# Performance work log

Measured on AMD Instinct MI355X. Metric: run time of the kernel, lower is better.

The kernel has to match this reference:

```python
import jax, jax.numpy as jnp
import numpy as np

NUM_HEADS = 8


def setup_inputs() -> dict:
    key = jax.random.key(0)
    ks = jax.random.split(key, 7)
    B, H, W, C = 1, 64, 64, 512
    x = jax.random.normal(ks[0], (B, H, W, C), dtype=jnp.float32)
    # lat in [-pi/2, pi/2), lon in [0, 2*pi) radians
    lat_grid = (jax.random.uniform(ks[1], (H, W), dtype=jnp.float32) - 0.5) * np.float32(np.pi)
    lon_grid = jax.random.uniform(ks[2], (H, W), dtype=jnp.float32) * np.float32(2 * np.pi)
    w_qkv = jax.random.normal(ks[3], (3 * C, C), dtype=jnp.float32) * 0.02
    b_qkv = jax.random.normal(ks[4], (3 * C,), dtype=jnp.float32) * 0.02
    w_out = jax.random.normal(ks[5], (C, C), dtype=jnp.float32) * 0.02
    b_out = jax.random.normal(ks[6], (C,), dtype=jnp.float32) * 0.02
    return {"x": x, "lat_grid": lat_grid, "lon_grid": lon_grid,
            "w_qkv": w_qkv, "b_qkv": b_qkv, "w_out": w_out, "b_out": b_out}


def _distance_bias(lat_grid, lon_grid):
    # Haversine great-circle distance between all pairs of grid points.
    lat = lat_grid.reshape(-1)  # [N]
    lon = lon_grid.reshape(-1)
    dlat = lat[None, :] - lat[:, None]  # [N, N]
    dlon = lon[None, :] - lon[:, None]
    a = jnp.sin(dlat / 2) ** 2 + jnp.cos(lat)[:, None] * jnp.cos(lat)[None, :] * jnp.sin(dlon / 2) ** 2
    dist = 2.0 * jnp.arcsin(jnp.sqrt(jnp.clip(a, 0.0, 1.0)))
    # torch .std() is unbiased (ddof=1)
    return -dist / jnp.std(dist, ddof=1)


def reference(x, lat_grid, lon_grid, w_qkv, b_qkv, w_out, b_out):
    B, H, W, C = x.shape
    nh = NUM_HEADS
    dh = C // nh
    N = H * W
    qkv = x @ w_qkv.T + b_qkv  # [B, H, W, 3C]
    qkv = qkv.reshape(B, N, 3, nh, dh)
    q = jnp.transpose(qkv[:, :, 0], (0, 2, 1, 3))  # [B, nh, N, dh]
    k = jnp.transpose(qkv[:, :, 1], (0, 2, 1, 3))
    v = jnp.transpose(qkv[:, :, 2], (0, 2, 1, 3))
    scale = np.float32(1.0 / np.sqrt(dh))
    attn = jnp.einsum("bhnd,bhmd->bhnm", q, k) * scale  # [B, nh, N, N]
    attn = attn + _distance_bias(lat_grid, lon_grid)[None, None]
    attn = jax.nn.softmax(attn, axis=-1)  # dropout is identity in eval
    out = jnp.einsum("bhnm,bhmd->bhnd", attn, v)  # [B, nh, N, dh]
    out = jnp.transpose(out, (0, 2, 1, 3)).reshape(B, H, W, C)
    return out @ w_out.T + b_out
```

## Files before the change

### kernel.cpp

```cpp
#include <hip/hip_runtime.h>
#include <hip/hip_bf16.h>


typedef __attribute__((ext_vector_type(8))) short bf16x8;
typedef __attribute__((ext_vector_type(4))) float f32x4;

#define MFMA16(a, b, c) __builtin_amdgcn_mfma_f32_16x16x32_bf16(a, b, c, 0, 0, 0)

__device__ __forceinline__ unsigned short f2b(float f) {
    union { float f; unsigned int i; } v;
    v.f = f;
    unsigned int lsb = (v.i >> 16) & 1u;
    unsigned int r = v.i + 0x7fffu + lsb;
    return (unsigned short)(r >> 16);
}

__global__ __launch_bounds__(256) void cvt_frag(
    const float* __restrict__ in, unsigned short* __restrict__ out) {
    int t = blockIdx.x * 256 + threadIdx.x;
    int l = t & 15, qd = (t >> 4) & 3, c = (t >> 6) & 15, g = t >> 10;
    const float* src = in + ((size_t)g * 16 + l) * 512 + c * 32 + qd * 8;
    float4 v0 = *(const float4*)src;
    float4 v1 = *(const float4*)(src + 4);
    ushort4 u0, u1;
    u0.x = f2b(v0.x); u0.y = f2b(v0.y); u0.z = f2b(v0.z); u0.w = f2b(v0.w);
    u1.x = f2b(v1.x); u1.y = f2b(v1.y); u1.z = f2b(v1.z); u1.w = f2b(v1.w);
    unsigned short* dst = out + (size_t)t * 8;
    *(ushort4*)dst = u0;
    *(ushort4*)(dst + 4) = u1;
}

__global__ __launch_bounds__(256) void dist_kernel(
    const float* __restrict__ lat, const float* __restrict__ lon,
    float* __restrict__ dist, double* __restrict__ partials) {
    __shared__ float sl_i[64], sc_i[64], so_i[64];
    __shared__ float sl_j[64], sc_j[64], so_j[64];
    __shared__ double rs[256], rs2[256];

    int bi = blockIdx.x;
    int i0 = (bi >> 6) << 6;
    int j0 = (bi & 63) << 6;
    int tid = threadIdx.x;

    if (tid < 64) {
        float la = lat[i0 + tid];
        sl_i[tid] = la; sc_i[tid] = __cosf(la); so_i[tid] = lon[i0 + tid];
    } else if (tid < 128) {
        int t = tid - 64;
        float la = lat[j0 + t];
        sl_j[t] = la; sc_j[t] = __cosf(la); so_j[t] = lon[j0 + t];
    }
    __syncthreads();

    double s = 0.0, s2 = 0.0;
    int col = tid & 63;
    int pcol = ((col & 15) << 2) + (col >> 4);
    float latj = sl_j[col], cj = sc_j[col], lonj = so_j[col];
#pragma unroll
    for (int kk = 0; kk < 16; kk++) {
        int row = (kk << 2) + (tid >> 6);
        float dlat = latj - sl_i[row];
        float dlon = lonj - so_i[row];
        float h1 = __sinf(0.5f * dlat);
        float h2 = __sinf(0.5f * dlon);
        float a = h1 * h1 + sc_i[row] * cj * h2 * h2;
        a = fminf(fmaxf(a, 0.0f), 1.0f);
        float d = 2.0f * asinf(sqrtf(a));
        dist[(size_t)(i0 + row) * 4096 + j0 + pcol] = d;
        s += (double)d;
        s2 += (double)d * (double)d;
    }
    rs[tid] = s; rs2[tid] = s2;
    __syncthreads();
    for (int off = 128; off > 0; off >>= 1) {
        if (tid < off) { rs[tid] += rs[tid + off]; rs2[tid] += rs2[tid + off]; }
        __syncthreads();
    }
    if (tid == 0) {
        partials[2 * bi] = rs[0];
        partials[2 * bi + 1] = rs2[0];
    }
}

__global__ __launch_bounds__(256) void stats_kernel(
    const double* __restrict__ partials, float* __restrict__ neg_inv_std) {
    __shared__ double rs[256], rs2[256];
    int tid = threadIdx.x;
    double s = 0.0, s2 = 0.0;
    for (int i = tid; i < 4096; i += 256) {
        s += partials[2 * i];
        s2 += partials[2 * i + 1];
    }
    rs[tid] = s; rs2[tid] = s2;
    __syncthreads();
    for (int off = 128; off > 0; off >>= 1) {
        if (tid < off) { rs[tid] += rs[tid + off]; rs2[tid] += rs2[tid + off]; }
        __syncthreads();
    }
    if (tid == 0) {
        double n = 16777216.0;
        double mean = rs[0] / n;
        double var = (rs2[0] - n * mean * mean) / (n - 1.0);
        *neg_inv_std = (float)(-1.0 / sqrt(var));
    }
}

__global__ __launch_bounds__(256) void qkv_gemm(
    const unsigned short* __restrict__ x, const unsigned short* __restrict__ w,
    const float* __restrict__ b,
    unsigned short* __restrict__ q, unsigned short* __restrict__ k,
    unsigned short* __restrict__ vt) {
    __shared__ unsigned short stage[64][72];
    int lane = threadIdx.x & 63, wave = threadIdx.x >> 6;
    int l16 = lane & 15, quad = lane >> 4;
    int m0 = blockIdx.y * 64 + wave * 16;
    int n0 = blockIdx.x * 64;

    const unsigned short* abase = x + (size_t)(blockIdx.y * 4 + wave) * 8192 + lane * 8;
    f32x4 acc[4];
#pragma unroll
    for (int nb = 0; nb < 4; nb++) acc[nb] = (f32x4){0.f, 0.f, 0.f, 0.f};

    for (int k0 = 0; k0 < 512; k0 += 32) {
        bf16x8 af = *(const bf16x8*)(abase + (k0 >> 5) * 512);
#pragma unroll
        for (int nb = 0; nb < 4; nb++) {
            bf16x8 bf = *(const bf16x8*)(w + (size_t)((n0 >> 4) + nb) * 8192
                                           + (k0 >> 5) * 512 + lane * 8);
            acc[nb] = MFMA16(af, bf, acc[nb]);
        }
    }
    if (blockIdx.x < 8) {
#pragma unroll
        for (int nb = 0; nb < 4; nb++) {
            int j = n0 + nb * 16 + l16;
            float bj = b[j];
            int h = j >> 6, d = j & 63;
#pragma unroll
            for (int r = 0; r < 4; r++) {
                int n = m0 + quad * 4 + r;
                q[((size_t)h * 4096 + n) * 64 + d] = f2b((acc[nb][r] + bj) * 0.125f);
            }
        }
    } else if (blockIdx.x < 16) {
        int h = blockIdx.x - 8;
#pragma unroll
        for (int nb = 0; nb < 4; nb++) {
            int d = nb * 16 + l16;
            float bj = b[512 + h * 64 + d];
#pragma unroll
            for (int r = 0; r < 4; r++)
                stage[wave * 16 + quad * 4 + r][d] = f2b(acc[nb][r] + bj);
        }
        __syncthreads();
        unsigned short* kb = k + ((size_t)h << 18) + (size_t)blockIdx.y * 4096;
#pragma unroll
        for (int p = 0; p < 2; p++) {
            int rid = p * 256 + threadIdx.x;
            int t = rid >> 7;
            int rem = rid & 127;
            int half = rem >> 6, qd = (rem >> 4) & 3, l = rem & 15;
            const unsigned short* src = &stage[t * 16 + l][half * 32 + qd * 8];
            unsigned short* dst = kb + t * 1024 + half * 512 + qd * 128 + l * 8;
            *(uint4*)dst = *(const uint4*)src;
        }
    } else {
        int h = blockIdx.x - 16;
#pragma unroll
        for (int nb = 0; nb < 4; nb++) {
            int d = nb * 16 + l16;
            float bj = b[1024 + h * 64 + d];
#pragma unroll
            for (int r = 0; r < 4; r++)
                stage[d][quad * 16 + r * 4 + wave] = f2b(acc[nb][r] + bj);
        }
        __syncthreads();
        int t = threadIdx.x;
        int d = t >> 2;
        int nq = (t & 3) * 16;
        unsigned short* dst = vt + ((size_t)h << 18) + (size_t)blockIdx.y * 4096
                            + (d >> 4) * 1024 + ((nq >> 5) & 1) * 512
                            + ((nq >> 3) & 3) * 128 + (d & 15) * 8;
        const unsigned short* src = &stage[d][nq];
        *(uint4*)dst = *(const uint4*)src;
        *(uint4*)(dst + 128) = *(const uint4*)(src + 8);
    }
}

__device__ __forceinline__ void attn_step(
    const unsigned short* __restrict__ kptr, const unsigned short* __restrict__ vtp,
    short* __restrict__ pb, int h, int kv0, int lane, int l16, int quad,
    bf16x8 qf0, bf16x8 qf1, float4 (&dv)[4], const float* __restrict__ drow,
    int kv_next, float nis, f32x4 (&o)[4], float (&lam)[4]) {
    size_t tbase = ((size_t)h << 18) + ((size_t)kv0 << 6) + lane * 8;
    const unsigned short* kb = kptr + tbase;
    const unsigned short* vb = vtp + tbase;
    f32x4 s[4];
#pragma unroll
    for (int cb = 0; cb < 4; cb++) {
        bf16x8 kf0 = *(const bf16x8*)(kb + cb * 1024);
        bf16x8 kf1 = *(const bf16x8*)(kb + cb * 1024 + 512);
        f32x4 z = (f32x4){0.f, 0.f, 0.f, 0.f};
        z = MFMA16(qf0, kf0, z);
        z = MFMA16(qf1, kf1, z);
        s[cb] = z;
    }
#pragma unroll
    for (int r = 0; r < 4; r++) {
        s[0][r] = fmaf(dv[r].x, nis, s[0][r]);
        s[1][r] = fmaf(dv[r].y, nis, s[1][r]);
        s[2][r] = fmaf(dv[r].z, nis, s[2][r]);
        s[3][r] = fmaf(dv[r].w, nis, s[3][r]);
    }
#pragma unroll
    for (int r = 0; r < 4; r++)
        dv[r] = *(const float4*)(drow + (size_t)r * 4096 + kv_next);
#pragma unroll
    for (int r = 0; r < 4; r++) {
        float p0 = __expf(s[0][r]);
        float p1 = __expf(s[1][r]);
        float p2 = __expf(s[2][r]);
        float p3 = __expf(s[3][r]);
        lam[r] += (p0 + p1) + (p2 + p3);
        unsigned int w0 = (unsigned int)f2b(p0) | ((unsigned int)f2b(p1) << 16);
        unsigned int w1 = (unsigned int)f2b(p2) | ((unsigned int)f2b(p3) << 16);
        uint2 pk; pk.x = w0; pk.y = w1;
        *(uint2*)(pb + (quad * 4 + r) * 72 + l16 * 4) = pk;
    }
    bf16x8 pf0 = *(const bf16x8*)(pb + l16 * 72 + quad * 8);
    bf16x8 pf1 = *(const bf16x8*)(pb + l16 * 72 + 32 + quad * 8);
#pragma unroll
    for (int db = 0; db < 4; db++) {
        bf16x8 vf0 = *(const bf16x8*)(vb + db * 1024);
        bf16x8 vf1 = *(const bf16x8*)(vb + db * 1024 + 512);
        o[db] = MFMA16(pf0, vf0, o[db]);
        o[db] = MFMA16(pf1, vf1, o[db]);
    }
}

__global__ __launch_bounds__(256, 6) void attn_kernel(
    const unsigned short* __restrict__ q, const unsigned short* __restrict__ k,
    const unsigned short* __restrict__ vt, const float* __restrict__ dist,
    const float* __restrict__ nis_p, unsigned short* __restrict__ att) {
    __shared__ __align__(16) char smem[9216];
    int tid = threadIdx.x;
    int lane = tid & 63, wave = tid >> 6;
    int l16 = lane & 15, quad = lane >> 4;
    int b = blockIdx.x;
    int h  = b & 7;
    int qs = b >> 3;
    int qt = wave;
    int q0 = qs * 16;
    int kvbase = qt * 1024;
    float nis = *nis_p;

    short* pb = (short*)smem + wave * 1152;

    const unsigned short* qbase = q + ((size_t)h * 4096 + q0 + l16) * 64 + quad * 8;
    bf16x8 qf0 = *(const bf16x8*)(qbase);
    bf16x8 qf1 = *(const bf16x8*)(qbase + 32);

    f32x4 o[4];
    float lam[4];
#pragma unroll
    for (int r = 0; r < 4; r++) {
        lam[r] = 0.f;
        o[0][r] = 0.f; o[1][r] = 0.f; o[2][r] = 0.f; o[3][r] = 0.f;
    }

    const float* drow = dist + (size_t)(q0 + quad * 4) * 4096 + l16 * 4;
    float4 dv[4];
#pragma unroll
    for (int r = 0; r < 4; r++)
        dv[r] = *(const float4*)(drow + (size_t)r * 4096 + kvbase);

    for (int it = 0; it < 16; ++it) {
        int kv0 = kvbase + it * 64;
        int kvn = (it == 15) ? kvbase : kv0 + 64;
        attn_step(k, vt, pb, h, kv0, lane, l16, quad, qf0, qf1, dv, drow, kvn,
                  nis, o, lam);
    }

#pragma unroll
    for (int r = 0; r < 4; r++)
#pragma unroll
        for (int off = 1; off < 16; off <<= 1)
            lam[r] += __shfl_xor(lam[r], off, 64);

    __syncthreads();
    float* obuf = (float*)smem;
    float* lbuf = (float*)(smem + 4096);
    if (l16 == 0)
#pragma unroll
        for (int r = 0; r < 4; r++)
            lbuf[qt * 16 + quad * 4 + r] = lam[r];
    if (qt == 0) {
#pragma unroll
        for (int db = 0; db < 4; db++)
#pragma unroll
            for (int r = 0; r < 4; r++)
                obuf[(quad * 4 + r) * 64 + db * 16 + l16] = o[db][r];
    }
    __syncthreads();
    if (qt == 1) {
#pragma unroll
        for (int db = 0; db < 4; db++)
#pragma unroll
            for (int r = 0; r < 4; r++)
                obuf[(quad * 4 + r) * 64 + db * 16 + l16] += o[db][r];
    }
    __syncthreads();
    if (qt == 2) {
#pragma unroll
        for (int db = 0; db < 4; db++)
#pragma unroll
            for (int r = 0; r < 4; r++)
                obuf[(quad * 4 + r) * 64 + db * 16 + l16] += o[db][r];
    }
    __syncthreads();
    if (qt == 3) {
#pragma unroll
        for (int db = 0; db < 4; db++)
#pragma unroll
            for (int r = 0; r < 4; r++)
                obuf[(quad * 4 + r) * 64 + db * 16 + l16] += o[db][r];
    }
    __syncthreads();

    int rl = tid >> 4;
    int d4 = (tid & 15) * 4;
    float L = lbuf[rl] + lbuf[16 + rl] + lbuf[32 + rl] + lbuf[48 + rl];
    float rinv = 1.0f / L;
    const float* ob = obuf + rl * 64 + d4;
    ushort4 ua;
    ua.x = f2b(ob[0] * rinv); ua.y = f2b(ob[1] * rinv);
    ua.z = f2b(ob[2] * rinv); ua.w = f2b(ob[3] * rinv);
    int row = q0 + rl;
    int col = h * 64 + d4;
    size_t dst = (size_t)(row >> 4) * 8192 + (col >> 5) * 512
               + ((col >> 3) & 3) * 128 + (row & 15) * 8 + (col & 7);
    *(ushort4*)(att + dst) = ua;
}

__global__ __launch_bounds__(256) void out_gemm(
    const unsigned short* __restrict__ att, const unsigned short* __restrict__ w,
    const float* __restrict__ b, float* __restrict__ out) {
    int lane = threadIdx.x & 63, wave = threadIdx.x >> 6;
    int l16 = lane & 15, quad = lane >> 4;
    int m0 = blockIdx.y * 64 + wave * 16;
    int n0 = blockIdx.x * 64;

    const unsigned short* abase = att + (size_t)(blockIdx.y * 4 + wave) * 8192 + lane * 8;
    f32x4 acc[4];
#pragma unroll
    for (int nb = 0; nb < 4; nb++) acc[nb] = (f32x4){0.f, 0.f, 0.f, 0.f};

    for (int k0 = 0; k0 < 512; k0 += 32) {
        bf16x8 af = *(const bf16x8*)(abase + (k0 >> 5) * 512);
#pragma unroll
        for (int nb = 0; nb < 4; nb++) {
            bf16x8 bf = *(const bf16x8*)(w + (size_t)((n0 >> 4) + nb) * 8192
                                           + (k0 >> 5) * 512 + lane * 8);
            acc[nb] = MFMA16(af, bf, acc[nb]);
        }
    }
#pragma unroll
    for (int nb = 0; nb < 4; nb++) {
        float bj = b[n0 + nb * 16 + l16];
#pragma unroll
        for (int r = 0; r < 4; r++)
            out[(size_t)(m0 + quad * 4 + r) * 512 + n0 + nb * 16 + l16] =
                acc[nb][r] + bj;
    }
}

extern "C" void kernel_launch(void* const* d_in, const int* in_sizes, int n_in,
                              void* d_out, int out_size, void* d_ws, size_t ws_size,
                              hipStream_t stream) {
    const float* x    = (const float*)d_in[0];
    const float* lat  = (const float*)d_in[1];
    const float* lon  = (const float*)d_in[2];
    const float* wqkv = (const float*)d_in[3];
    const float* bqkv = (const float*)d_in[4];
    const float* wout = (const float*)d_in[5];
    const float* bout = (const float*)d_in[6];
    float* out = (float*)d_out;

    char* ws = (char*)d_ws;
    float* dist        = (float*)ws;
    double* partials   = (double*)(ws + 67108864);
    float* nis         = (float*)(ws + 67108864 + 65536);
    unsigned short* q  = (unsigned short*)(ws + 67108864 + 65600);
    unsigned short* k  = q  + (size_t)8 * 4096 * 64;
    unsigned short* vt = k  + (size_t)8 * 4096 * 64;
    unsigned short* att = vt + (size_t)8 * 4096 * 64;
    unsigned short* xb  = att + (size_t)4096 * 512;
    unsigned short* wqb = xb  + (size_t)4096 * 512;
    unsigned short* wob = wqb + (size_t)1536 * 512;

    cvt_frag<<<1024, 256, 0, stream>>>(x, xb);
    cvt_frag<<<384, 256, 0, stream>>>(wqkv, wqb);
    cvt_frag<<<128, 256, 0, stream>>>(wout, wob);
    dist_kernel<<<4096, 256, 0, stream>>>(lat, lon, dist, partials);
    stats_kernel<<<1, 256, 0, stream>>>(partials, nis);
    qkv_gemm<<<dim3(24, 64), 256, 0, stream>>>(xb, wqb, bqkv, q, k, vt);
    attn_kernel<<<2048, 256, 0, stream>>>(q, k, vt, dist, nis, att);
    out_gemm<<<dim3(8, 64), 256, 0, stream>>>(att, wob, bout, out);
}
```

Baseline: 262.5 us.

## Process 32 query rows per attention block to reuse K/V fragments

Each wave in the attention kernel now computes two 16-row query tiles against the same K and V fragments, which halves K/V global loads per query and halves the grid to 1024 blocks. Block indices are remapped so that blocks sharing a head land on the same XCD, aiming for better L2 locality of K/V. This doubles accumulator and LDS usage per block, and the occupancy hint drops from 6 to 3, so there is less latency hiding. The epilogue now writes 8 columns per thread.

```diff
diff --git a/kernel.cpp b/kernel.cpp
--- a/kernel.cpp
+++ b/kernel.cpp
@@ -187,15 +187,18 @@
     }
 }
 
-__device__ __forceinline__ void attn_step(
+__device__ __forceinline__ void attn_step32(
     const unsigned short* __restrict__ kptr, const unsigned short* __restrict__ vtp,
     short* __restrict__ pb, int h, int kv0, int lane, int l16, int quad,
-    bf16x8 qf0, bf16x8 qf1, float4 (&dv)[4], const float* __restrict__ drow,
-    int kv_next, float nis, f32x4 (&o)[4], float (&lam)[4]) {
+    bf16x8 qf0, bf16x8 qf1, bf16x8 qf2, bf16x8 qf3,
+    float4 (&dvL)[4], float4 (&dvH)[4],
+    const float* __restrict__ drowL, const float* __restrict__ drowH,
+    int kv_next, float nis,
+    f32x4 (&oL)[4], f32x4 (&oH)[4], float (&lamL)[4], float (&lamH)[4]) {
     size_t tbase = ((size_t)h << 18) + ((size_t)kv0 << 6) + lane * 8;
     const unsigned short* kb = kptr + tbase;
     const unsigned short* vb = vtp + tbase;
-    f32x4 s[4];
+    f32x4 sl[4], sh[4];
 #pragma unroll
     for (int cb = 0; cb < 4; cb++) {
         bf16x8 kf0 = *(const bf16x8*)(kb + cb * 1024);
@@ -203,143 +206,189 @@
         f32x4 z = (f32x4){0.f, 0.f, 0.f, 0.f};
         z = MFMA16(qf0, kf0, z);
         z = MFMA16(qf1, kf1, z);
-        s[cb] = z;
+        sl[cb] = z;
+        f32x4 y = (f32x4){0.f, 0.f, 0.f, 0.f};
+        y = MFMA16(qf2, kf0, y);
+        y = MFMA16(qf3, kf1, y);
+        sh[cb] = y;
     }
 #pragma unroll
     for (int r = 0; r < 4; r++) {
-        s[0][r] = fmaf(dv[r].x, nis, s[0][r]);
-        s[1][r] = fmaf(dv[r].y, nis, s[1][r]);
-        s[2][r] = fmaf(dv[r].z, nis, s[2][r]);
-        s[3][r] = fmaf(dv[r].w, nis, s[3][r]);
-    }
-#pragma unroll
-    for (int r = 0; r < 4; r++)
-        dv[r] = *(const float4*)(drow + (size_t)r * 4096 + kv_next);
+        sl[0][r] = fmaf(dvL[r].x, nis, sl[0][r]);
+        sl[1][r] = fmaf(dvL[r].y, nis, sl[1][r]);
+        sl[2][r] = fmaf(dvL[r].z, nis, sl[2][r]);
+        sl[3][r] = fmaf(dvL[r].w, nis, sl[3][r]);
+        sh[0][r] = fmaf(dvH[r].x, nis, sh[0][r]);
+        sh[1][r] = fmaf(dvH[r].y, nis, sh[1][r]);
+        sh[2][r] = fmaf(dvH[r].z, nis, sh[2][r]);
+        sh[3][r] = fmaf(dvH[r].w, nis, sh[3][r]);
+    }
 #pragma unroll
     for (int r = 0; r < 4; r++) {
-        float p0 = __expf(s[0][r]);
-        float p1 = __expf(s[1][r]);
-        float p2 = __expf(s[2][r]);
-        float p3 = __expf(s[3][r]);
-        lam[r] += (p0 + p1) + (p2 + p3);
-        unsigned int w0 = (unsigned int)f2b(p0) | ((unsigned int)f2b(p1) << 16);
-        unsigned int w1 = (unsigned int)f2b(p2) | ((unsigned int)f2b(p3) << 16);
-        uint2 pk; pk.x = w0; pk.y = w1;
+        float p0 = __expf(sl[0][r]);
+        float p1 = __expf(sl[1][r]);
+        float p2 = __expf(sl[2][r]);
+        float p3 = __expf(sl[3][r]);
+        lamL[r] += (p0 + p1) + (p2 + p3);
+        uint2 pk;
+        pk.x = (unsigned int)f2b(p0) | ((unsigned int)f2b(p1) << 16);
+        pk.y = (unsigned int)f2b(p2) | ((unsigned int)f2b(p3) << 16);
         *(uint2*)(pb + (quad * 4 + r) * 72 + l16 * 4) = pk;
+        float h0 = __expf(sh[0][r]);
+        float h1 = __expf(sh[1][r]);
+        float h2 = __expf(sh[2][r]);
+        float h3 = __expf(sh[3][r]);
+        lamH[r] += (h0 + h1) + (h2 + h3);
+        uint2 ph;
+        ph.x = (unsigned int)f2b(h0) | ((unsigned int)f2b(h1) << 16);
+        ph.y = (unsigned int)f2b(h2) | ((unsigned int)f2b(h3) << 16);
+        *(uint2*)(pb + (16 + quad * 4 + r) * 72 + l16 * 4) = ph;
+    }
+#pragma unroll
+    for (int r = 0; r < 4; r++) {
+        dvL[r] = *(const float4*)(drowL + (size_t)r * 4096 + kv_next);
+        dvH[r] = *(const float4*)(drowH + (size_t)r * 4096 + kv_next);
     }
     bf16x8 pf0 = *(const bf16x8*)(pb + l16 * 72 + quad * 8);
     bf16x8 pf1 = *(const bf16x8*)(pb + l16 * 72 + 32 + quad * 8);
+    bf16x8 pf2 = *(const bf16x8*)(pb + (16 + l16) * 72 + quad * 8);
+    bf16x8 pf3 = *(const bf16x8*)(pb + (16 + l16) * 72 + 32 + quad * 8);
 #pragma unroll
     for (int db = 0; db < 4; db++) {
         bf16x8 vf0 = *(const bf16x8*)(vb + db * 1024);
         bf16x8 vf1 = *(const bf16x8*)(vb + db * 1024 + 512);
-        o[db] = MFMA16(pf0, vf0, o[db]);
-        o[db] = MFMA16(pf1, vf1, o[db]);
-    }
-}
-
-__global__ __launch_bounds__(256, 6) void attn_kernel(
+        oL[db] = MFMA16(pf0, vf0, oL[db]);
+        oL[db] = MFMA16(pf1, vf1, oL[db]);
+        oH[db] = MFMA16(pf2, vf0, oH[db]);
+        oH[db] = MFMA16(pf3, vf1, oH[db]);
+    }
+}
+
+__global__ __launch_bounds__(256, 3) void attn_kernel(
     const unsigned short* __restrict__ q, const unsigned short* __restrict__ k,
     const unsigned short* __restrict__ vt, const float* __restrict__ dist,
     const float* __restrict__ nis_p, unsigned short* __restrict__ att) {
-    __shared__ __align__(16) char smem[9216];
+    __shared__ __align__(16) char smem[18432];
     int tid = threadIdx.x;
     int lane = tid & 63, wave = tid >> 6;
     int l16 = lane & 15, quad = lane >> 4;
     int b = blockIdx.x;
-    int h  = b & 7;
-    int qs = b >> 3;
+    int xcd = b & 7, j = b >> 3;
+    int h  = (xcd & 3) * 2 + (j & 1);
+    int qs = (xcd >> 2) * 64 + (j >> 1);
     int qt = wave;
-    int q0 = qs * 16;
+    int q0 = qs * 32;
     int kvbase = qt * 1024;
     float nis = *nis_p;
 
-    short* pb = (short*)smem + wave * 1152;
+    short* pb = (short*)smem + wave * 2304;
 
     const unsigned short* qbase = q + ((size_t)h * 4096 + q0 + l16) * 64 + quad * 8;
     bf16x8 qf0 = *(const bf16x8*)(qbase);
     bf16x8 qf1 = *(const bf16x8*)(qbase + 32);
-
-    f32x4 o[4];
-    float lam[4];
+    const unsigned short* qbase2 = qbase + 16 * 64;
+    bf16x8 qf2 = *(const bf16x8*)(qbase2);
+    bf16x8 qf3 = *(const bf16x8*)(qbase2 + 32);
+
+    f32x4 oL[4], oH[4];
+    float lamL[4], lamH[4];
 #pragma unroll
     for (int r = 0; r < 4; r++) {
-        lam[r] = 0.f;
-        o[0][r] = 0.f; o[1][r] = 0.f; o[2][r] = 0.f; o[3][r] = 0.f;
-    }
-
-    const float* drow = dist + (size_t)(q0 + quad * 4) * 4096 + l16 * 4;
-    float4 dv[4];
-#pragma unroll
-    for (int r = 0; r < 4; r++)
-        dv[r] = *(const float4*)(drow + (size_t)r * 4096 + kvbase);
+        lamL[r] = 0.f; lamH[r] = 0.f;
+        oL[0][r] = 0.f; oL[1][r] = 0.f; oL[2][r] = 0.f; oL[3][r] = 0.f;
+        oH[0][r] = 0.f; oH[1][r] = 0.f; oH[2][r] = 0.f; oH[3][r] = 0.f;
+    }
+
+    const float* drowL = dist + (size_t)(q0 + quad * 4) * 4096 + l16 * 4;
+    const float* drowH = drowL + (size_t)16 * 4096;
+    float4 dvL[4], dvH[4];
+#pragma unroll
+    for (int r = 0; r < 4; r++) {
+        dvL[r] = *(const float4*)(drowL + (size_t)r * 4096 + kvbase);
+        dvH[r] = *(const float4*)(drowH + (size_t)r * 4096 + kvbase);
+    }
 
     for (int it = 0; it < 16; ++it) {
         int kv0 = kvbase + it * 64;
         int kvn = (it == 15) ? kvbase : kv0 + 64;
-        attn_step(k, vt, pb, h, kv0, lane, l16, quad, qf0, qf1, dv, drow, kvn,
-                  nis, o, lam);
+        attn_step32(k, vt, pb, h, kv0, lane, l16, quad, qf0, qf1, qf2, qf3,
+                    dvL, dvH, drowL, drowH, kvn, nis, oL, oH, lamL, lamH);
     }
 
 #pragma unroll
     for (int r = 0; r < 4; r++)
 #pragma unroll
-        for (int off = 1; off < 16; off <<= 1)
-            lam[r] += __shfl_xor(lam[r], off, 64);
+        for (int off = 1; off < 16; off <<= 1) {
+            lamL[r] += __shfl_xor(lamL[r], off, 64);
+            lamH[r] += __shfl_xor(lamH[r], off, 64);
+        }
 
     __syncthreads();
     float* obuf = (float*)smem;
-    float* lbuf = (float*)(smem + 4096);
+    float* lbuf = (float*)(smem + 8192);
     if (l16 == 0)
 #pragma unroll
-        for (int r = 0; r < 4; r++)
-            lbuf[qt * 16 + quad * 4 + r] = lam[r];
+        for (int r = 0; r < 4; r++) {
+            lbuf[qt * 32 + quad * 4 + r] = lamL[r];
+            lbuf[qt * 32 + 16 + quad * 4 + r] = lamH[r];
+        }
     if (qt == 0) {
 #pragma unroll
         for (int db = 0; db < 4; db++)
 #pragma unroll
-            for (int r = 0; r < 4; r++)
-                obuf[(quad * 4 + r) * 64 + db * 16 + l16] = o[db][r];
+            for (int r = 0; r < 4; r++) {
+                obuf[(quad * 4 + r) * 64 + db * 16 + l16] = oL[db][r];
+                obuf[(16 + quad * 4 + r) * 64 + db * 16 + l16] = oH[db][r];
+            }
     }
     __syncthreads();
     if (qt == 1) {
 #pragma unroll
         for (int db = 0; db < 4; db++)
 #pragma unroll
-            for (int r = 0; r < 4; r++)
-                obuf[(quad * 4 + r) * 64 + db * 16 + l16] += o[db][r];
+            for (int r = 0; r < 4; r++) {
+                obuf[(quad * 4 + r) * 64 + db * 16 + l16] += oL[db][r];
+                obuf[(16 + quad * 4 + r) * 64 + db * 16 + l16] += oH[db][r];
+            }
     }
     __syncthreads();
     if (qt == 2) {
 #pragma unroll
         for (int db = 0; db < 4; db++)
 #pragma unroll
-            for (int r = 0; r < 4; r++)
-                obuf[(quad * 4 + r) * 64 + db * 16 + l16] += o[db][r];
+            for (int r = 0; r < 4; r++) {
+                obuf[(quad * 4 + r) * 64 + db * 16 + l16] += oL[db][r];
+                obuf[(16 + quad * 4 + r) * 64 + db * 16 + l16] += oH[db][r];
+            }
     }
     __syncthreads();
     if (qt == 3) {
 #pragma unroll
         for (int db = 0; db < 4; db++)
 #pragma unroll
-            for (int r = 0; r < 4; r++)
-                obuf[(quad * 4 + r) * 64 + db * 16 + l16] += o[db][r];
-    }
-    __syncthreads();
-
-    int rl = tid >> 4;
-    int d4 = (tid & 15) * 4;
-    float L = lbuf[rl] + lbuf[16 + rl] + lbuf[32 + rl] + lbuf[48 + rl];
+            for (int r = 0; r < 4; r++) {
+                obuf[(quad * 4 + r) * 64 + db * 16 + l16] += oL[db][r];
+                obuf[(16 + quad * 4 + r) * 64 + db * 16 + l16] += oH[db][r];
+            }
+    }
+    __syncthreads();
+
+    int rl = tid >> 3;
+    int d8 = (tid & 7) * 8;
+    float L = lbuf[rl] + lbuf[32 + rl] + lbuf[64 + rl] + lbuf[96 + rl];
     float rinv = 1.0f / L;
-    const float* ob = obuf + rl * 64 + d4;
-    ushort4 ua;
+    const float* ob = obuf + rl * 64 + d8;
+    ushort4 ua, ub;
     ua.x = f2b(ob[0] * rinv); ua.y = f2b(ob[1] * rinv);
     ua.z = f2b(ob[2] * rinv); ua.w = f2b(ob[3] * rinv);
+    ub.x = f2b(ob[4] * rinv); ub.y = f2b(ob[5] * rinv);
+    ub.z = f2b(ob[6] * rinv); ub.w = f2b(ob[7] * rinv);
     int row = q0 + rl;
-    int col = h * 64 + d4;
+    int col = h * 64 + d8;
     size_t dst = (size_t)(row >> 4) * 8192 + (col >> 5) * 512
                + ((col >> 3) & 3) * 128 + (row & 15) * 8 + (col & 7);
     *(ushort4*)(att + dst) = ua;
+    *(ushort4*)(att + dst + 4) = ub;
 }
 
 __global__ __launch_bounds__(256) void out_gemm(
@@ -404,6 +453,6 @@
     dist_kernel<<<4096, 256, 0, stream>>>(lat, lon, dist, partials);
     stats_kernel<<<1, 256, 0, stream>>>(partials, nis);
     qkv_gemm<<<dim3(24, 64), 256, 0, stream>>>(xb, wqb, bqkv, q, k, vt);
-    attn_kernel<<<2048, 256, 0, stream>>>(q, k, vt, dist, nis, att);
+    attn_kernel<<<1024, 256, 0, stream>>>(q, k, vt, dist, nis, att);
     out_gemm<<<dim3(8, 64), 256, 0, stream>>>(att, wob, bout, out);
 }
```

Result: slower. 281.7 us (+7.3%).
